# Kernel optimization log

Measured on AMD Instinct MI355X. Metric: run time of the kernel, lower is better.

Reference implementation:

```python
import jax, jax.numpy as jnp
import numpy as np
from jax import lax

B, T, D_IN, H, K, A = 32, 512, 42, 800, 20, 20  # batch, seq, d_in, hidden, linear_out, alphabet_size

def _lstm_dir(x, wih, whh, b, reverse):
    # x: [T,B,D]; wih: [4H,D]; whh: [4H,H]; b: [4H] (b_ih+b_hh merged; mathematically identical)
    xg = jnp.einsum('tbd,hd->tbh', x, wih) + b
    if reverse:
        xg = xg[::-1]
    nh = whh.shape[1]
    h0 = jnp.zeros((x.shape[1], nh), x.dtype)
    def step(carry, xt):
        h, c = carry
        g = xt + h @ whh.T
        i, f, gg, o = jnp.split(g, 4, axis=-1)  # torch gate order i,f,g,o
        c = jax.nn.sigmoid(f) * c + jax.nn.sigmoid(i) * jnp.tanh(gg)
        h = jax.nn.sigmoid(o) * jnp.tanh(c)
        return (h, c), h
    _, hs = lax.scan(step, (h0, h0), xg)
    return hs[::-1] if reverse else hs

_BOND_LENS = jnp.array([145.801, 152.326, 132.868], jnp.float32)  # N-CA, CA-C, C-N (pm)
_BOND_ANGS = jnp.array([2.124, 1.941, 2.028], jnp.float32)

def _coords(tors):
    # tors: [T,B,3] dihedrals -> NeRF-style recursive backbone placement (3 atoms/residue)
    bsz = tors.shape[1]
    a0 = jnp.broadcast_to(jnp.array([0., 0., 1.], jnp.float32), (bsz, 3))
    b0 = jnp.broadcast_to(jnp.array([0., 1., 1.], jnp.float32), (bsz, 3))
    c0 = jnp.broadcast_to(jnp.array([1., 1., 1.], jnp.float32), (bsz, 3))
    def step(carry, tor):
        a, b, c = carry
        outs = []
        for i in range(3):  # three backbone atoms per residue
            r, t, p = _BOND_LENS[i], _BOND_ANGS[i], tor[:, i]
            d2 = jnp.stack([-r * jnp.cos(t) * jnp.ones_like(p),
                            r * jnp.cos(p) * jnp.sin(t),
                            r * jnp.sin(p) * jnp.sin(t)], axis=1)
            bc = c - b
            bc = bc / jnp.linalg.norm(bc, axis=1, keepdims=True)
            n = jnp.cross(b - a, bc)
            n = n / jnp.linalg.norm(n, axis=1, keepdims=True)
            m = jnp.stack([bc, jnp.cross(n, bc), n], axis=2)  # [B,3,3] local frame
            d = jnp.einsum('bij,bj->bi', m, d2) + c
            outs.append(d)
            a, b, c = b, c, d
        return (a, b, c), jnp.stack(outs)
    _, new = lax.scan(step, (a0, b0, c0), tors)  # [T,3,B,3]
    init3 = jnp.stack([a0, b0, c0])
    return jnp.concatenate([init3, new.reshape(-1, bsz, 3)], axis=0)  # [3+3T,B,3]

def _forward(x, wih_l0_f, whh_l0_f, b_l0_f, wih_l0_b, whh_l0_b, b_l0_b,
             wih_l1_f, whh_l1_f, b_l1_f, wih_l1_b, whh_l1_b, b_l1_b,
             lin_w, lin_b, alphabet):
    xs = jnp.transpose(x, (1, 0, 2))  # torch: x.float().transpose(0,1) -> [T,B,D]
    h1 = jnp.concatenate([_lstm_dir(xs, wih_l0_f, whh_l0_f, b_l0_f, False),
                          _lstm_dir(xs, wih_l0_b, whh_l0_b, b_l0_b, True)], axis=-1)
    h2 = jnp.concatenate([_lstm_dir(h1, wih_l1_f, whh_l1_f, b_l1_f, False),
                          _lstm_dir(h1, wih_l1_b, whh_l1_b, b_l1_b, True)], axis=-1)  # [T,B,2H]
    logits = h2 @ lin_w.T + lin_b  # [T,B,K]
    p = jax.nn.softmax(logits, axis=1)  # faithful to nn.Softmax(dim=1) on 3D input (over batch)
    ang = jnp.arctan2(p @ jnp.sin(alphabet), p @ jnp.cos(alphabet))  # [T,B,3] angular mixture
    return _coords(ang)

def setup_inputs():
    key = jax.random.key(0)
    ks = jax.random.split(key, 16)
    s = 0.05
    return {
        'x': jax.random.normal(ks[0], (B, T, D_IN), jnp.float32),
        'wih_l0_f': jax.random.normal(ks[1], (4 * H, D_IN), jnp.float32) * s,
        'whh_l0_f': jax.random.normal(ks[2], (4 * H, H), jnp.float32) * s,
        'b_l0_f': jax.random.normal(ks[3], (4 * H,), jnp.float32) * s,
        'wih_l0_b': jax.random.normal(ks[4], (4 * H, D_IN), jnp.float32) * s,
        'whh_l0_b': jax.random.normal(ks[5], (4 * H, H), jnp.float32) * s,
        'b_l0_b': jax.random.normal(ks[6], (4 * H,), jnp.float32) * s,
        'wih_l1_f': jax.random.normal(ks[7], (4 * H, 2 * H), jnp.float32) * s,
        'whh_l1_f': jax.random.normal(ks[8], (4 * H, H), jnp.float32) * s,
        'b_l1_f': jax.random.normal(ks[9], (4 * H,), jnp.float32) * s,
        'wih_l1_b': jax.random.normal(ks[10], (4 * H, 2 * H), jnp.float32) * s,
        'whh_l1_b': jax.random.normal(ks[11], (4 * H, H), jnp.float32) * s,
        'b_l1_b': jax.random.normal(ks[12], (4 * H,), jnp.float32) * s,
        'lin_w': jax.random.normal(ks[13], (K, 2 * H), jnp.float32) * s,
        'lin_b': jax.random.normal(ks[14], (K,), jnp.float32) * s,
        'alphabet': jax.random.uniform(ks[15], (A, 3), jnp.float32, -np.pi, np.pi),
    }

def reference(x, wih_l0_f, whh_l0_f, b_l0_f, wih_l0_b, whh_l0_b, b_l0_b,
              wih_l1_f, whh_l1_f, b_l1_f, wih_l1_b, whh_l1_b, b_l1_b,
              lin_w, lin_b, alphabet):
    return _forward(x, wih_l0_f, whh_l0_f, b_l0_f, wih_l0_b, whh_l0_b, b_l0_b,
                    wih_l1_f, whh_l1_f, b_l1_f, wih_l1_b, whh_l1_b, b_l1_b,
                    lin_w, lin_b, alphabet)
```

## Files before the change

### kernel.cpp

```cpp
#include <hip/hip_runtime.h>

typedef unsigned short u16;
typedef _Float16 f16x8 __attribute__((ext_vector_type(8)));
typedef float f32x4 __attribute__((ext_vector_type(4)));

#define T_LEN 512
#define BATCH 32
#define DIN 42
#define XPAD 64
#define HID 800
#define G4 3200
#define KCLS 20
#define NBLK 100
#define WSCAN 16
#define HSTR 1664
#define BOFF 832
#define KPAD 1632

__device__ __forceinline__ u16 f2h(float f){
    union { _Float16 h; u16 u; } v; v.h = (_Float16)f; return v.u;
}
__device__ __forceinline__ float sigm(float x){ return 1.f / (1.f + __expf(-x)); }
__device__ __forceinline__ float tanh_(float x){ return 2.f / (1.f + __expf(-2.f * x)) - 1.f; }

__global__ void k_cvt(const float* __restrict__ s, u16* __restrict__ d, int n){
    for (int i = blockIdx.x * blockDim.x + threadIdx.x; i < n; i += gridDim.x * blockDim.x)
        d[i] = f2h(s[i]);
}
__global__ void k_zero16(u16* __restrict__ d, int n){
    for (int i = blockIdx.x * blockDim.x + threadIdx.x; i < n; i += gridDim.x * blockDim.x)
        d[i] = 0;
}
__global__ void k_xT(const float* __restrict__ x, u16* __restrict__ xT){
    const int n = T_LEN * BATCH * XPAD;
    for (int i = blockIdx.x * blockDim.x + threadIdx.x; i < n; i += gridDim.x * blockDim.x){
        int t = i / (BATCH * XPAD);
        int rem = i % (BATCH * XPAD);
        int b = rem / XPAD, k = rem % XPAD;
        xT[i] = (k < DIN) ? f2h(x[((size_t)b * T_LEN + t) * DIN + k]) : (u16)0;
    }
}
__global__ void k_pack2(const float* __restrict__ whh, const float* __restrict__ wih,
                        int nkk, int kin, u16* __restrict__ P2){
    const int n_use = 50 * 2 * nkk * 2 * 64 * 8;
    for (int i = blockIdx.x * blockDim.x + threadIdx.x; i < n_use; i += gridDim.x * blockDim.x){
        int e = i & 7;
        int lane = (i >> 3) & 63;
        int which = (i >> 9) & 1;
        int r = i >> 10;
        int kk = r % nkk;
        int tn = r / nkk;
        int nh = tn & 1, tile = tn >> 1;
        int lr = lane & 15, kgrp = lane >> 4;
        int col = nh * 32 + which * 16 + lr;
        int gate = col >> 4, j = tile * 16 + (col & 15);
        float v;
        if (kk < 25){
            int k = kk * 32 + kgrp * 8 + e;
            v = whh[(size_t)(gate * 800 + j) * 800 + k];
        } else {
            int xk = (kk - 25) * 32 + kgrp * 8 + e;
            v = (xk < kin) ? wih[(size_t)(gate * 800 + j) * kin + xk] : 0.f;
        }
        P2[i] = f2h(v);
    }
}
__global__ void k_pack_bias(const float* __restrict__ b, float* __restrict__ bpk){
    for (int i = blockIdx.x * blockDim.x + threadIdx.x; i < G4; i += gridDim.x * blockDim.x){
        int g = i & 3, j = i >> 2;
        bpk[i] = b[g * 800 + j];
    }
}

__global__ __launch_bounds__(256) void mfma_gemm(
    const u16* __restrict__ A0, const u16* __restrict__ A1, int lda,
    const void* __restrict__ B0_, const void* __restrict__ B1_, int ldb,
    const float* __restrict__ bias0, const float* __restrict__ bias1,
    void* __restrict__ C0, void* __restrict__ C1, int ldc,
    int M, int N, int K, int outmode, int b_is_f32, int khole)
{
    __shared__ u16 At[128 * 40];
    __shared__ u16 Bt[128 * 40];
    const int z = blockIdx.z;
    const u16* Ag = z ? A1 : A0;
    const void* Bg_ = z ? B1_ : B0_;
    const float* bias = z ? bias1 : bias0;
    void* Cg = z ? C1 : C0;
    const u16*   Bu = (const u16*)Bg_;
    const float* Bf = (const float*)Bg_;
    const int tid = threadIdx.x;
    const int lane = tid & 63, w = tid >> 6;
    const int wr = w >> 1, wc = w & 1;
    const int lr = lane & 15, kb8 = (lane >> 4) * 8;
    const int m0 = blockIdx.y * 128, n0 = blockIdx.x * 128;
    const int sr = tid >> 1, skg = (tid & 1) << 4;
    f32x4 acc[4][4] = {};
    const int KT = (K + 31) >> 5;
    for (int kt = 0; kt < KT; ++kt){
        const int k0 = kt << 5;
        __syncthreads();
        {
            size_t base = (size_t)(m0 + sr) * lda + k0 + skg;
            const f16x8* p = (const f16x8*)(Ag + base);
            *(f16x8*)&At[sr * 40 + skg] = p[0];
            *(f16x8*)&At[sr * 40 + skg + 8] = p[1];
        }
        {
            int rn = n0 + sr;
            const int hole = khole && (k0 == 800);
            const int kb = (khole && k0 >= 832) ? (k0 - 32) : k0;
            if (rn < N && !hole && b_is_f32){
                size_t base = (size_t)rn * ldb + kb + skg;
                const float4* p = (const float4*)(Bf + base);
                float4 q0 = p[0], q1 = p[1], q2 = p[2], q3 = p[3];
                f16x8 v0, v1;
                v0[0] = (_Float16)q0.x; v0[1] = (_Float16)q0.y; v0[2] = (_Float16)q0.z; v0[3] = (_Float16)q0.w;
                v0[4] = (_Float16)q1.x; v0[5] = (_Float16)q1.y; v0[6] = (_Float16)q1.z; v0[7] = (_Float16)q1.w;
                v1[0] = (_Float16)q2.x; v1[1] = (_Float16)q2.y; v1[2] = (_Float16)q2.z; v1[3] = (_Float16)q2.w;
                v1[4] = (_Float16)q3.x; v1[5] = (_Float16)q3.y; v1[6] = (_Float16)q3.z; v1[7] = (_Float16)q3.w;
                *(f16x8*)&Bt[sr * 40 + skg] = v0;
                *(f16x8*)&Bt[sr * 40 + skg + 8] = v1;
            } else if (rn < N && !hole){
                size_t base = (size_t)rn * ldb + kb + skg;
                const f16x8* p = (const f16x8*)(Bu + base);
                *(f16x8*)&Bt[sr * 40 + skg] = p[0];
                *(f16x8*)&Bt[sr * 40 + skg + 8] = p[1];
            } else {
                f16x8 zv = {};
                *(f16x8*)&Bt[sr * 40 + skg] = zv;
                *(f16x8*)&Bt[sr * 40 + skg + 8] = zv;
            }
        }
        __syncthreads();
        f16x8 af[4], bfr[4];
        #pragma unroll
        for (int mi = 0; mi < 4; ++mi)
            af[mi] = *(const f16x8*)&At[(wr * 64 + mi * 16 + lr) * 40 + kb8];
        #pragma unroll
        for (int ni = 0; ni < 4; ++ni)
            bfr[ni] = *(const f16x8*)&Bt[(wc * 64 + ni * 16 + lr) * 40 + kb8];
        #pragma unroll
        for (int mi = 0; mi < 4; ++mi)
            #pragma unroll
            for (int ni = 0; ni < 4; ++ni)
                acc[mi][ni] = __builtin_amdgcn_mfma_f32_16x16x32_f16(af[mi], bfr[ni], acc[mi][ni], 0, 0, 0);
    }
    #pragma unroll
    for (int mi = 0; mi < 4; ++mi){
        #pragma unroll
        for (int ni = 0; ni < 4; ++ni){
            int col = n0 + wc * 64 + ni * 16 + lr;
            if (col >= N) continue;
            float bs = bias ? bias[col] : 0.f;
            int pc = (outmode == 2) ? ((col % 800) * 4 + col / 800) : col;
            #pragma unroll
            for (int r = 0; r < 4; ++r){
                int row = m0 + wr * 64 + mi * 16 + ((lane >> 4) * 4 + r);
                float v = acc[mi][ni][r] + bs;
                if (outmode) ((u16*)Cg)[(size_t)row * ldc + pc] = f2h(v);
                else         ((float*)Cg)[(size_t)row * ldc + pc] = v;
            }
        }
    }
}

__global__ __launch_bounds__(256, 1) void scan_coop(
    int nkk, int W, int s0,
    const u16* __restrict__ xTp,
    const u16* __restrict__ xgF, const u16* __restrict__ xgB,
    const u16* __restrict__ P2f, const u16* __restrict__ P2b,
    const float* __restrict__ bpkF, const float* __restrict__ bpkB,
    const u16* __restrict__ hzero, u16* __restrict__ h,
    float* __restrict__ cF, float* __restrict__ cB,
    int cload, int cstore, unsigned* __restrict__ arrive)
{
    __shared__ u16 wlds[2 * 27 * 2 * 64 * 8];
    __shared__ float gLds[32][65];
    const int tid = threadIdx.x;
    const int dir = blockIdx.x & 1;
    const int tile = blockIdx.x >> 1;
    const u16* P2  = dir ? P2b : P2f;
    const u16* xg  = dir ? xgB : xgF;
    const float* bpk = dir ? bpkB : bpkF;
    float* cst = dir ? cB : cF;

    const int wcnt = 2 * nkk * 2 * 64 * 8;
    {
        const u16* src = P2 + (size_t)tile * wcnt;
        for (int i = tid * 8; i < wcnt; i += 256 * 8)
            *(f16x8*)&wlds[i] = *(const f16x8*)&src[i];
    }
    __syncthreads();

    const int lane = tid & 63, w = tid >> 6;
    const int mi = w >> 1, nh = w & 1;
    const int lr = lane & 15, kb8 = (lane >> 4) * 8;
    const int arow = mi * 16 + lr;
    const int b_ep = tid >> 3;
    const int up   = (tid & 7) * 2;
    const int j    = tile * 16 + up;

    float c0 = 0.f, c1 = 0.f;
    if (cload){
        c0 = cst[tile * 512 + tid * 2];
        c1 = cst[tile * 512 + tid * 2 + 1];
    }
    f32x4 bb0 = {}, bb1 = {};
    if (nkk == 27){
        bb0 = *(const f32x4*)(bpk + j * 4);
        bb1 = *(const f32x4*)(bpk + j * 4 + 4);
    }

    const size_t hstep = (size_t)BATCH * HSTR;

    for (int q = 0; q < W; ++q){
        const int s = s0 + q;
        const int t = dir ? (T_LEN - 1 - s) : s;
        const u16* hprev = (s == 0) ? (hzero + dir * BOFF)
                           : (h + (size_t)(dir ? t + 1 : t - 1) * hstep + dir * BOFF);

        const u16* hp = hprev + (size_t)arow * HSTR + kb8;
        f16x8 areg[25];
        #pragma unroll
        for (int kk = 0; kk < 25; ++kk)
            areg[kk] = *(const f16x8*)(hp + kk * 32);
        f16x8 xa0 = {}, xa1 = {}, xv = {};
        if (nkk == 27){
            const u16* xt = xTp + (size_t)t * (BATCH * XPAD) + arow * XPAD + kb8;
            xa0 = *(const f16x8*)(xt);
            xa1 = *(const f16x8*)(xt + 32);
        } else {
            const int qq = dir ? (W - 1 - q) : q;
            xv = *(const f16x8*)(xg + ((size_t)qq * BATCH + b_ep) * G4 + j * 4);
        }

        f32x4 a0a = {}, a0b = {}, a1a = {}, a1b = {};
        #pragma unroll
        for (int kk = 0; kk < 24; kk += 2){
            f16x8 b0e = *(const f16x8*)&wlds[(size_t)((nh * nkk + kk) * 2 + 0) * 512 + lane * 8];
            f16x8 b1e = *(const f16x8*)&wlds[(size_t)((nh * nkk + kk) * 2 + 1) * 512 + lane * 8];
            f16x8 b0o = *(const f16x8*)&wlds[(size_t)((nh * nkk + kk + 1) * 2 + 0) * 512 + lane * 8];
            f16x8 b1o = *(const f16x8*)&wlds[(size_t)((nh * nkk + kk + 1) * 2 + 1) * 512 + lane * 8];
            a0a = __builtin_amdgcn_mfma_f32_16x16x32_f16(areg[kk],     b0e, a0a, 0, 0, 0);
            a1a = __builtin_amdgcn_mfma_f32_16x16x32_f16(areg[kk],     b1e, a1a, 0, 0, 0);
            a0b = __builtin_amdgcn_mfma_f32_16x16x32_f16(areg[kk + 1], b0o, a0b, 0, 0, 0);
            a1b = __builtin_amdgcn_mfma_f32_16x16x32_f16(areg[kk + 1], b1o, a1b, 0, 0, 0);
        }
        {
            f16x8 b0e = *(const f16x8*)&wlds[(size_t)((nh * nkk + 24) * 2 + 0) * 512 + lane * 8];
            f16x8 b1e = *(const f16x8*)&wlds[(size_t)((nh * nkk + 24) * 2 + 1) * 512 + lane * 8];
            a0a = __builtin_amdgcn_mfma_f32_16x16x32_f16(areg[24], b0e, a0a, 0, 0, 0);
            a1a = __builtin_amdgcn_mfma_f32_16x16x32_f16(areg[24], b1e, a1a, 0, 0, 0);
        }
        if (nkk == 27){
            f16x8 b0e = *(const f16x8*)&wlds[(size_t)((nh * nkk + 25) * 2 + 0) * 512 + lane * 8];
            f16x8 b1e = *(const f16x8*)&wlds[(size_t)((nh * nkk + 25) * 2 + 1) * 512 + lane * 8];
            a0b = __builtin_amdgcn_mfma_f32_16x16x32_f16(xa0, b0e, a0b, 0, 0, 0);
            a1b = __builtin_amdgcn_mfma_f32_16x16x32_f16(xa0, b1e, a1b, 0, 0, 0);
            f16x8 b0o = *(const f16x8*)&wlds[(size_t)((nh * nkk + 26) * 2 + 0) * 512 + lane * 8];
            f16x8 b1o = *(const f16x8*)&wlds[(size_t)((nh * nkk + 26) * 2 + 1) * 512 + lane * 8];
            a0a = __builtin_amdgcn_mfma_f32_16x16x32_f16(xa1, b0o, a0a, 0, 0, 0);
            a1a = __builtin_amdgcn_mfma_f32_16x16x32_f16(xa1, b1o, a1a, 0, 0, 0);
        }
        f32x4 acc0 = a0a + a0b;
        f32x4 acc1 = a1a + a1b;
        #pragma unroll
        for (int r = 0; r < 4; ++r){
            int b = mi * 16 + (lane >> 4) * 4 + r;
            gLds[b][nh * 32 + lr]      = acc0[r];
            gLds[b][nh * 32 + 16 + lr] = acc1[r];
        }
        __syncthreads();

        {
            float gi0, gf0, gg0, go0, gi1, gf1, gg1, go1;
            if (nkk == 27){
                gi0 = gLds[b_ep][up]          + bb0[0];
                gf0 = gLds[b_ep][16 + up]     + bb0[1];
                gg0 = gLds[b_ep][32 + up]     + bb0[2];
                go0 = gLds[b_ep][48 + up]     + bb0[3];
                gi1 = gLds[b_ep][up + 1]      + bb1[0];
                gf1 = gLds[b_ep][16 + up + 1] + bb1[1];
                gg1 = gLds[b_ep][32 + up + 1] + bb1[2];
                go1 = gLds[b_ep][48 + up + 1] + bb1[3];
            } else {
                gi0 = gLds[b_ep][up]          + (float)xv[0];
                gf0 = gLds[b_ep][16 + up]     + (float)xv[1];
                gg0 = gLds[b_ep][32 + up]     + (float)xv[2];
                go0 = gLds[b_ep][48 + up]     + (float)xv[3];
                gi1 = gLds[b_ep][up + 1]      + (float)xv[4];
                gf1 = gLds[b_ep][16 + up + 1] + (float)xv[5];
                gg1 = gLds[b_ep][32 + up + 1] + (float)xv[6];
                go1 = gLds[b_ep][48 + up + 1] + (float)xv[7];
            }
            float cn0 = sigm(gf0) * c0 + sigm(gi0) * tanh_(gg0);
            float cn1 = sigm(gf1) * c1 + sigm(gi1) * tanh_(gg1);
            c0 = cn0; c1 = cn1;
            union { unsigned u; _Float16 hh[2]; } pk;
            pk.hh[0] = (_Float16)(sigm(go0) * tanh_(cn0));
            pk.hh[1] = (_Float16)(sigm(go1) * tanh_(cn1));
            unsigned* dst = (unsigned*)(h + (size_t)t * hstep + dir * BOFF + (size_t)b_ep * HSTR + j);
            __hip_atomic_store(dst, pk.u, __ATOMIC_RELAXED, __HIP_MEMORY_SCOPE_AGENT);
        }

        if (q != W - 1){
            const unsigned tgt = (unsigned)(s + 1);
            __syncthreads();
            if (tid == 0)
                __hip_atomic_store(arrive + (size_t)blockIdx.x * 32, tgt,
                                   __ATOMIC_RELAXED, __HIP_MEMORY_SCOPE_AGENT);
            if (tid < 64){
                const unsigned* slot = arrive + (size_t)(((tid < 50) ? tid : 0) * 2 + dir) * 32;
                while (true){
                    unsigned v = __hip_atomic_load(slot, __ATOMIC_RELAXED, __HIP_MEMORY_SCOPE_AGENT);
                    if (__all((int)(v >= tgt))) break;
                    __builtin_amdgcn_s_sleep(1);
                }
            }
            __syncthreads();
        }
    }
    if (cstore){
        cst[tile * 512 + tid * 2]     = c0;
        cst[tile * 512 + tid * 2 + 1] = c1;
    }
}

__global__ __launch_bounds__(64) void k_smax_ang(
    const float* __restrict__ logits, const float* __restrict__ alphabet,
    float* __restrict__ ang)
{
    int t = blockIdx.x;
    __shared__ float P[32][20];
    __shared__ float sA[20][3], cA[20][3];
    int tid = threadIdx.x;
    for (int idx = tid; idx < 32 * 20; idx += 64){
        int b = idx / 20, k = idx % 20;
        P[b][k] = logits[((size_t)t * 32 + b) * 20 + k];
    }
    for (int idx = tid; idx < 60; idx += 64){
        float al = alphabet[idx];
        sA[idx / 3][idx % 3] = sinf(al);
        cA[idx / 3][idx % 3] = cosf(al);
    }
    __syncthreads();
    if (tid < 20){
        float mx = -1e30f;
        for (int b = 0; b < 32; ++b) mx = fmaxf(mx, P[b][tid]);
        float s = 0.f;
        for (int b = 0; b < 32; ++b){ float e = __expf(P[b][tid] - mx); P[b][tid] = e; s += e; }
        float inv = 1.f / s;
        for (int b = 0; b < 32; ++b) P[b][tid] *= inv;
    }
    __syncthreads();
    if (tid < 32){
        float sx = 0, sy = 0, sz = 0, cx = 0, cy = 0, cz = 0;
        for (int k = 0; k < 20; ++k){
            float p = P[tid][k];
            sx += p * sA[k][0]; sy += p * sA[k][1]; sz += p * sA[k][2];
            cx += p * cA[k][0]; cy += p * cA[k][1]; cz += p * cA[k][2];
        }
        size_t base = ((size_t)t * 32 + tid) * 3;
        ang[base + 0] = atan2f(sx, cx);
        ang[base + 1] = atan2f(sy, cy);
        ang[base + 2] = atan2f(sz, cz);
    }
}

__global__ __launch_bounds__(64) void k_coords(const float* __restrict__ ang, float* __restrict__ out){
    int b = threadIdx.x;
    if (b >= 32) return;
    float ax = 0.f, ay = 0.f, az = 1.f;
    float bx = 0.f, by = 1.f, bz = 1.f;
    float cx = 1.f, cy = 1.f, cz = 1.f;
    out[(0 * 32 + b) * 3 + 0] = ax; out[(0 * 32 + b) * 3 + 1] = ay; out[(0 * 32 + b) * 3 + 2] = az;
    out[(1 * 32 + b) * 3 + 0] = bx; out[(1 * 32 + b) * 3 + 1] = by; out[(1 * 32 + b) * 3 + 2] = bz;
    out[(2 * 32 + b) * 3 + 0] = cx; out[(2 * 32 + b) * 3 + 1] = cy; out[(2 * 32 + b) * 3 + 2] = cz;
    const float rr[3] = {145.801f, 152.326f, 132.868f};
    const float ba[3] = {2.124f, 1.941f, 2.028f};
    float ct[3], st[3];
    #pragma unroll
    for (int i = 0; i < 3; ++i){ ct[i] = cosf(ba[i]); st[i] = sinf(ba[i]); }
    for (int t = 0; t < T_LEN; ++t){
        #pragma unroll
        for (int i = 0; i < 3; ++i){
            float p = ang[((size_t)t * 32 + b) * 3 + i];
            float d2x = -rr[i] * ct[i];
            float d2y = rr[i] * cosf(p) * st[i];
            float d2z = rr[i] * sinf(p) * st[i];
            float bcx = cx - bx, bcy = cy - by, bcz = cz - bz;
            float inb = 1.f / sqrtf(bcx * bcx + bcy * bcy + bcz * bcz);
            bcx *= inb; bcy *= inb; bcz *= inb;
            float ux = bx - ax, uy = by - ay, uz = bz - az;
            float nx = uy * bcz - uz * bcy;
            float ny = uz * bcx - ux * bcz;
            float nz = ux * bcy - uy * bcx;
            float inn = 1.f / sqrtf(nx * nx + ny * ny + nz * nz);
            nx *= inn; ny *= inn; nz *= inn;
            float mx = ny * bcz - nz * bcy;
            float my = nz * bcx - nx * bcz;
            float mz = nx * bcy - ny * bcx;
            float dx = bcx * d2x + mx * d2y + nx * d2z + cx;
            float dy = bcy * d2x + my * d2y + ny * d2z + cy;
            float dz = bcz * d2x + mz * d2y + nz * d2z + cz;
            int row = 3 + t * 3 + i;
            out[((size_t)row * 32 + b) * 3 + 0] = dx;
            out[((size_t)row * 32 + b) * 3 + 1] = dy;
            out[((size_t)row * 32 + b) * 3 + 2] = dz;
            ax = bx; ay = by; az = bz;
            bx = cx; by = cy; bz = cz;
            cx = dx; cy = dy; cz = dz;
        }
    }
}

extern "C" void kernel_launch(void* const* d_in, const int* in_sizes, int n_in,
                              void* d_out, int out_size, void* d_ws, size_t ws_size,
                              hipStream_t stream)
{
    const float* x     = (const float*)d_in[0];
    const float* wih0f = (const float*)d_in[1];
    const float* whh0f = (const float*)d_in[2];
    const float* b0f   = (const float*)d_in[3];
    const float* wih0b = (const float*)d_in[4];
    const float* whh0b = (const float*)d_in[5];
    const float* b0b   = (const float*)d_in[6];
    const float* wih1f = (const float*)d_in[7];
    const float* whh1f = (const float*)d_in[8];
    const float* b1f   = (const float*)d_in[9];
    const float* wih1b = (const float*)d_in[10];
    const float* whh1b = (const float*)d_in[11];
    const float* b1b   = (const float*)d_in[12];
    const float* linw  = (const float*)d_in[13];
    const float* linb  = (const float*)d_in[14];
    const float* alpha = (const float*)d_in[15];
    (void)in_sizes; (void)n_in; (void)out_size; (void)ws_size;

    char* ws = (char*)d_ws;
    size_t off = 0;
    auto alloc = [&](size_t bytes) -> void* {
        off = (off + 255) & ~(size_t)255;
        void* p = ws + off;
        off += bytes;
        return p;
    };
    u16* xT     = (u16*)alloc((size_t)T_LEN * BATCH * XPAD * 2);
    u16* h1     = (u16*)alloc((size_t)T_LEN * BATCH * HSTR * 2);
    u16* h2     = (u16*)alloc((size_t)T_LEN * BATCH * HSTR * 2);
    u16* P2_0f  = (u16*)alloc((size_t)50 * 2 * 27 * 2 * 64 * 8 * 2);
    u16* P2_0b  = (u16*)alloc((size_t)50 * 2 * 27 * 2 * 64 * 8 * 2);
    u16* P2_1f  = (u16*)alloc((size_t)50 * 2 * 25 * 2 * 64 * 8 * 2);
    u16* P2_1b  = (u16*)alloc((size_t)50 * 2 * 25 * 2 * 64 * 8 * 2);
    u16* linwB  = (u16*)alloc((size_t)KCLS * 1600 * 2);
    float* bpk0f = (float*)alloc((size_t)G4 * 4);
    float* bpk0b = (float*)alloc((size_t)G4 * 4);
    u16* hzero  = (u16*)alloc((size_t)BATCH * HSTR * 2);
    float* c1f  = (float*)alloc((size_t)50 * 512 * 4);
    float* c1b  = (float*)alloc((size_t)50 * 512 * 4);
    u16* xgFc   = (u16*)alloc((size_t)WSCAN * BATCH * G4 * 2);
    u16* xgBc   = (u16*)alloc((size_t)WSCAN * BATCH * G4 * 2);
    unsigned* arrive = (unsigned*)alloc((size_t)NBLK * 32 * 4);
    float* logitsF = (float*)xgFc;
    float* angF    = (float*)xgBc;

    k_zero16<<<dim3(32), dim3(256), 0, stream>>>(hzero, BATCH * HSTR);
    k_cvt<<<dim3(64), dim3(256), 0, stream>>>(linw, linwB, KCLS * 1600);
    k_xT<<<dim3(512), dim3(256), 0, stream>>>(x, xT);
    k_pack2<<<dim3(1024), dim3(256), 0, stream>>>(whh0f, wih0f, 27, DIN, P2_0f);
    k_pack2<<<dim3(1024), dim3(256), 0, stream>>>(whh0b, wih0b, 27, DIN, P2_0b);
    k_pack2<<<dim3(1024), dim3(256), 0, stream>>>(whh1f, nullptr, 25, 0, P2_1f);
    k_pack2<<<dim3(1024), dim3(256), 0, stream>>>(whh1b, nullptr, 25, 0, P2_1b);
    k_pack_bias<<<dim3(8), dim3(256), 0, stream>>>(b0f, bpk0f);
    k_pack_bias<<<dim3(8), dim3(256), 0, stream>>>(b0b, bpk0b);

    const size_t hstep = (size_t)BATCH * HSTR;

    hipMemsetAsync(arrive, 0, (size_t)NBLK * 32 * 4, stream);
    scan_coop<<<dim3(NBLK), dim3(256), 0, stream>>>(
        27, T_LEN, 0,
        xT, nullptr, nullptr,
        P2_0f, P2_0b, bpk0f, bpk0b,
        hzero, h1, nullptr, nullptr, 0, 0, arrive);

    hipMemsetAsync(arrive, 0, (size_t)NBLK * 32 * 4, stream);
    for (int w = 0; w < T_LEN / WSCAN; ++w){
        const int s0  = w * WSCAN;
        const int t0f = s0;
        const int t0b = T_LEN - (w + 1) * WSCAN;
        mfma_gemm<<<dim3(G4 / 128, WSCAN * BATCH / 128, 2), dim3(256), 0, stream>>>(
            h1 + (size_t)t0f * hstep, h1 + (size_t)t0b * hstep, HSTR,
            wih1f, wih1b, 1600, b1f, b1b,
            xgFc, xgBc, G4, WSCAN * BATCH, G4, KPAD, 2, 1, 1);
        scan_coop<<<dim3(NBLK), dim3(256), 0, stream>>>(
            25, WSCAN, s0,
            nullptr, xgFc, xgBc,
            P2_1f, P2_1b, nullptr, nullptr,
            hzero, h2, c1f, c1b, (w > 0) ? 1 : 0, 1, arrive);
    }

    mfma_gemm<<<dim3(1, T_LEN * BATCH / 128, 1), dim3(256), 0, stream>>>(
        h2, h2, HSTR, linwB, linwB, 1600, linb, linb,
        logitsF, logitsF, KCLS, T_LEN * BATCH, KCLS, KPAD, 0, 0, 1);

    k_smax_ang<<<dim3(T_LEN), dim3(64), 0, stream>>>(logitsF, alpha, angF);
    k_coords<<<dim3(1), dim3(64), 0, stream>>>(angF, (float*)d_out);
}
```

Baseline: 8.163 ms.

## Fuse layer-1 input projection into a single persistent 200-block scan kernel

Replaces the layer-1 loop, which alternated a windowed input-projection GEMM with short cooperative scan launches, with one persistent kernel. The new kernel keeps both the recurrent and input weights for 8 hidden units per block resident in LDS and computes the h1 projection inside each step before waiting on the barrier. It uses 200 blocks instead of 100, cutting per-block recurrent work and letting the h1 part overlap the cross-block wait. In exchange it launches many fewer kernels, but each step now does three times the MFMA work in the loop and the flag barrier has to span more blocks.

Result: slower. 9.063 ms (+11.0%).

```diff
diff --git a/kernel.cpp b/kernel.cpp
--- a/kernel.cpp
+++ b/kernel.cpp
@@ -12,7 +12,6 @@
 #define G4 3200
 #define KCLS 20
 #define NBLK 100
-#define WSCAN 16
 #define HSTR 1664
 #define BOFF 832
 #define KPAD 1632
@@ -62,6 +61,28 @@
             int xk = (kk - 25) * 32 + kgrp * 8 + e;
             v = (xk < kin) ? wih[(size_t)(gate * 800 + j) * kin + xk] : 0.f;
         }
+        P2[i] = f2h(v);
+    }
+}
+__global__ void k_pack_l1(const float* __restrict__ whh1, const float* __restrict__ wih1,
+                          u16* __restrict__ P2){
+    const int n = 100 * 2 * 75 * 512;
+    for (int i = blockIdx.x * blockDim.x + threadIdx.x; i < n; i += gridDim.x * blockDim.x){
+        int e = i & 7;
+        int lane = (i >> 3) & 63;
+        int rem = i >> 9;
+        int kk = rem % 75;
+        int r = rem / 75;
+        int wv = r & 1, tile = r >> 1;
+        int lr = lane & 15, kgrp = lane >> 4;
+        int col = wv * 16 + lr;
+        int g = col & 3, u = col >> 2;
+        int j = tile * 8 + u;
+        int krel = kgrp * 8 + e;
+        float v;
+        if (kk < 25)      v = whh1[(size_t)(g * 800 + j) * 800 + kk * 32 + krel];
+        else if (kk < 50) v = wih1[(size_t)(g * 800 + j) * 1600 + (kk - 25) * 32 + krel];
+        else              v = wih1[(size_t)(g * 800 + j) * 1600 + 800 + (kk - 50) * 32 + krel];
         P2[i] = f2h(v);
     }
 }
@@ -167,12 +188,10 @@
 __global__ __launch_bounds__(256, 1) void scan_coop(
     int nkk, int W, int s0,
     const u16* __restrict__ xTp,
-    const u16* __restrict__ xgF, const u16* __restrict__ xgB,
     const u16* __restrict__ P2f, const u16* __restrict__ P2b,
     const float* __restrict__ bpkF, const float* __restrict__ bpkB,
     const u16* __restrict__ hzero, u16* __restrict__ h,
-    float* __restrict__ cF, float* __restrict__ cB,
-    int cload, int cstore, unsigned* __restrict__ arrive)
+    unsigned* __restrict__ arrive)
 {
     __shared__ u16 wlds[2 * 27 * 2 * 64 * 8];
     __shared__ float gLds[32][65];
@@ -180,9 +199,7 @@
     const int dir = blockIdx.x & 1;
     const int tile = blockIdx.x >> 1;
     const u16* P2  = dir ? P2b : P2f;
-    const u16* xg  = dir ? xgB : xgF;
     const float* bpk = dir ? bpkB : bpkF;
-    float* cst = dir ? cB : cF;
 
     const int wcnt = 2 * nkk * 2 * 64 * 8;
     {
@@ -201,15 +218,8 @@
     const int j    = tile * 16 + up;
 
     float c0 = 0.f, c1 = 0.f;
-    if (cload){
-        c0 = cst[tile * 512 + tid * 2];
-        c1 = cst[tile * 512 + tid * 2 + 1];
-    }
-    f32x4 bb0 = {}, bb1 = {};
-    if (nkk == 27){
-        bb0 = *(const f32x4*)(bpk + j * 4);
-        bb1 = *(const f32x4*)(bpk + j * 4 + 4);
-    }
+    f32x4 bb0 = *(const f32x4*)(bpk + j * 4);
+    f32x4 bb1 = *(const f32x4*)(bpk + j * 4 + 4);
 
     const size_t hstep = (size_t)BATCH * HSTR;
 
@@ -224,14 +234,11 @@
         #pragma unroll
         for (int kk = 0; kk < 25; ++kk)
             areg[kk] = *(const f16x8*)(hp + kk * 32);
-        f16x8 xa0 = {}, xa1 = {}, xv = {};
-        if (nkk == 27){
+        f16x8 xa0, xa1;
+        {
             const u16* xt = xTp + (size_t)t * (BATCH * XPAD) + arow * XPAD + kb8;
             xa0 = *(const f16x8*)(xt);
             xa1 = *(const f16x8*)(xt + 32);
-        } else {
-            const int qq = dir ? (W - 1 - q) : q;
-            xv = *(const f16x8*)(xg + ((size_t)qq * BATCH + b_ep) * G4 + j * 4);
         }
 
         f32x4 a0a = {}, a0b = {}, a1a = {}, a1b = {};
@@ -252,7 +259,7 @@
             a0a = __builtin_amdgcn_mfma_f32_16x16x32_f16(areg[24], b0e, a0a, 0, 0, 0);
             a1a = __builtin_amdgcn_mfma_f32_16x16x32_f16(areg[24], b1e, a1a, 0, 0, 0);
         }
-        if (nkk == 27){
+        {
             f16x8 b0e = *(const f16x8*)&wlds[(size_t)((nh * nkk + 25) * 2 + 0) * 512 + lane * 8];
             f16x8 b1e = *(const f16x8*)&wlds[(size_t)((nh * nkk + 25) * 2 + 1) * 512 + lane * 8];
             a0b = __builtin_amdgcn_mfma_f32_16x16x32_f16(xa0, b0e, a0b, 0, 0, 0);
@@ -273,26 +280,14 @@
         __syncthreads();
 
         {
-            float gi0, gf0, gg0, go0, gi1, gf1, gg1, go1;
-            if (nkk == 27){
-                gi0 = gLds[b_ep][up]          + bb0[0];
-                gf0 = gLds[b_ep][16 + up]     + bb0[1];
-                gg0 = gLds[b_ep][32 + up]     + bb0[2];
-                go0 = gLds[b_ep][48 + up]     + bb0[3];
-                gi1 = gLds[b_ep][up + 1]      + bb1[0];
-                gf1 = gLds[b_ep][16 + up + 1] + bb1[1];
-                gg1 = gLds[b_ep][32 + up + 1] + bb1[2];
-                go1 = gLds[b_ep][48 + up + 1] + bb1[3];
-            } else {
-                gi0 = gLds[b_ep][up]          + (float)xv[0];
-                gf0 = gLds[b_ep][16 + up]     + (float)xv[1];
-                gg0 = gLds[b_ep][32 + up]     + (float)xv[2];
-                go0 = gLds[b_ep][48 + up]     + (float)xv[3];
-                gi1 = gLds[b_ep][up + 1]      + (float)xv[4];
-                gf1 = gLds[b_ep][16 + up + 1] + (float)xv[5];
-                gg1 = gLds[b_ep][32 + up + 1] + (float)xv[6];
-                go1 = gLds[b_ep][48 + up + 1] + (float)xv[7];
-            }
+            float gi0 = gLds[b_ep][up]          + bb0[0];
+            float gf0 = gLds[b_ep][16 + up]     + bb0[1];
+            float gg0 = gLds[b_ep][32 + up]     + bb0[2];
+            float go0 = gLds[b_ep][48 + up]     + bb0[3];
+            float gi1 = gLds[b_ep][up + 1]      + bb1[0];
+            float gf1 = gLds[b_ep][16 + up + 1] + bb1[1];
+            float gg1 = gLds[b_ep][32 + up + 1] + bb1[2];
+            float go1 = gLds[b_ep][48 + up + 1] + bb1[3];
             float cn0 = sigm(gf0) * c0 + sigm(gi0) * tanh_(gg0);
             float cn1 = sigm(gf1) * c1 + sigm(gi1) * tanh_(gg1);
             c0 = cn0; c1 = cn1;
@@ -320,9 +315,114 @@
             __syncthreads();
         }
     }
-    if (cstore){
-        cst[tile * 512 + tid * 2]     = c0;
-        cst[tile * 512 + tid * 2 + 1] = c1;
+}
+
+__global__ __launch_bounds__(256, 1) void scan_l1(
+    const u16* __restrict__ P2f, const u16* __restrict__ P2b,
+    const float* __restrict__ bpkF, const float* __restrict__ bpkB,
+    const u16* __restrict__ h1, const u16* __restrict__ hzero,
+    u16* __restrict__ h2, unsigned* __restrict__ arrive)
+{
+    __shared__ u16 wlds[2 * 75 * 512];
+    __shared__ float gLds[32][36];
+    const int tid = threadIdx.x;
+    const int dir = blockIdx.x & 1;
+    const int tile = blockIdx.x >> 1;
+    const u16* P2 = dir ? P2b : P2f;
+    const float* bpk = dir ? bpkB : bpkF;
+
+    {
+        const u16* src = P2 + (size_t)tile * (2 * 75 * 512);
+        for (int i = tid * 8; i < 2 * 75 * 512; i += 256 * 8)
+            *(f16x8*)&wlds[i] = *(const f16x8*)&src[i];
+    }
+    __syncthreads();
+
+    const int lane = tid & 63, w = tid >> 6;
+    const int mi = w >> 1, wv = w & 1;
+    const int lr = lane & 15, kb8 = (lane >> 4) * 8;
+    const int arow = mi * 16 + lr;
+    const int b_ep = tid >> 3, u_ep = tid & 7;
+    const int j = tile * 8 + u_ep;
+    const f32x4 bb = *(const f32x4*)(bpk + j * 4);
+    float cc = 0.f;
+    const size_t hstep = (size_t)BATCH * HSTR;
+    const u16* wl = wlds + (size_t)wv * 75 * 512 + (size_t)lane * 8;
+
+    for (int s = 0; s < T_LEN; ++s){
+        const int t = dir ? (T_LEN - 1 - s) : s;
+        f32x4 aA = {}, aB = {};
+        const u16* h1row = h1 + (size_t)t * hstep + (size_t)arow * HSTR;
+        {
+            f16x8 a[25];
+            #pragma unroll
+            for (int k = 0; k < 25; ++k) a[k] = *(const f16x8*)(h1row + k * 32 + kb8);
+            #pragma unroll
+            for (int k = 0; k < 25; ++k){
+                f16x8 bw = *(const f16x8*)(wl + (size_t)(25 + k) * 512);
+                if (k & 1) aB = __builtin_amdgcn_mfma_f32_16x16x32_f16(a[k], bw, aB, 0, 0, 0);
+                else       aA = __builtin_amdgcn_mfma_f32_16x16x32_f16(a[k], bw, aA, 0, 0, 0);
+            }
+        }
+        {
+            f16x8 a[25];
+            #pragma unroll
+            for (int k = 0; k < 25; ++k) a[k] = *(const f16x8*)(h1row + BOFF + k * 32 + kb8);
+            #pragma unroll
+            for (int k = 0; k < 25; ++k){
+                f16x8 bw = *(const f16x8*)(wl + (size_t)(50 + k) * 512);
+                if (k & 1) aB = __builtin_amdgcn_mfma_f32_16x16x32_f16(a[k], bw, aB, 0, 0, 0);
+                else       aA = __builtin_amdgcn_mfma_f32_16x16x32_f16(a[k], bw, aA, 0, 0, 0);
+            }
+        }
+        if (s > 0){
+            const unsigned tgt = (unsigned)s;
+            if (tid < 128){
+                int slot = (tid < 100) ? tid : 99;
+                const unsigned* sp = arrive + (size_t)(slot * 2 + dir) * 32;
+                while (true){
+                    unsigned v = __hip_atomic_load(sp, __ATOMIC_RELAXED, __HIP_MEMORY_SCOPE_AGENT);
+                    if (__all((int)(v >= tgt))) break;
+                    __builtin_amdgcn_s_sleep(1);
+                }
+            }
+            __syncthreads();
+        }
+        {
+            const u16* hp = (s == 0) ? (hzero + dir * BOFF + (size_t)arow * HSTR)
+                : (h2 + (size_t)(dir ? t + 1 : t - 1) * hstep + dir * BOFF + (size_t)arow * HSTR);
+            f16x8 a[25];
+            #pragma unroll
+            for (int k = 0; k < 25; ++k) a[k] = *(const f16x8*)(hp + k * 32 + kb8);
+            #pragma unroll
+            for (int k = 0; k < 25; ++k){
+                f16x8 bw = *(const f16x8*)(wl + (size_t)k * 512);
+                if (k & 1) aB = __builtin_amdgcn_mfma_f32_16x16x32_f16(a[k], bw, aB, 0, 0, 0);
+                else       aA = __builtin_amdgcn_mfma_f32_16x16x32_f16(a[k], bw, aA, 0, 0, 0);
+            }
+        }
+        f32x4 acc = aA + aB;
+        #pragma unroll
+        for (int r = 0; r < 4; ++r)
+            gLds[mi * 16 + (lane >> 4) * 4 + r][wv * 16 + lr] = acc[r];
+        __syncthreads();
+        {
+            float gi = gLds[b_ep][u_ep * 4 + 0] + bb[0];
+            float gf = gLds[b_ep][u_ep * 4 + 1] + bb[1];
+            float gg = gLds[b_ep][u_ep * 4 + 2] + bb[2];
+            float go = gLds[b_ep][u_ep * 4 + 3] + bb[3];
+            float cn = sigm(gf) * cc + sigm(gi) * tanh_(gg);
+            cc = cn;
+            u16 hv = f2h(sigm(go) * tanh_(cn));
+            u16* dst = h2 + (size_t)t * hstep + dir * BOFF + (size_t)b_ep * HSTR + j;
+            __hip_atomic_store(dst, hv, __ATOMIC_RELAXED, __HIP_MEMORY_SCOPE_AGENT);
+        }
+        if (s != T_LEN - 1){
+            __syncthreads();
+            if (tid == 0)
+                __hip_atomic_store(arrive + (size_t)blockIdx.x * 32, (unsigned)(s + 1),
+                                   __ATOMIC_RELAXED, __HIP_MEMORY_SCOPE_AGENT);
+        }
     }
 }
 
@@ -444,59 +544,43 @@
         off += bytes;
         return p;
     };
-    u16* xT     = (u16*)alloc((size_t)T_LEN * BATCH * XPAD * 2);
-    u16* h1     = (u16*)alloc((size_t)T_LEN * BATCH * HSTR * 2);
-    u16* h2     = (u16*)alloc((size_t)T_LEN * BATCH * HSTR * 2);
-    u16* P2_0f  = (u16*)alloc((size_t)50 * 2 * 27 * 2 * 64 * 8 * 2);
-    u16* P2_0b  = (u16*)alloc((size_t)50 * 2 * 27 * 2 * 64 * 8 * 2);
-    u16* P2_1f  = (u16*)alloc((size_t)50 * 2 * 25 * 2 * 64 * 8 * 2);
-    u16* P2_1b  = (u16*)alloc((size_t)50 * 2 * 25 * 2 * 64 * 8 * 2);
+    u16* xT   = (u16*)alloc((size_t)T_LEN * BATCH * XPAD * 2);
+    u16* h1   = (u16*)alloc((size_t)T_LEN * BATCH * HSTR * 2);
+    u16* h2   = (u16*)alloc((size_t)T_LEN * BATCH * HSTR * 2);
+    u16* Wbig = (u16*)alloc((size_t)2 * 7680000 * 2);
+    u16* P2_0f  = Wbig;
+    u16* P2_0b  = Wbig + 2764800;
+    u16* P2L1f  = Wbig;
+    u16* P2L1b  = Wbig + 7680000;
     u16* linwB  = (u16*)alloc((size_t)KCLS * 1600 * 2);
     float* bpk0f = (float*)alloc((size_t)G4 * 4);
     float* bpk0b = (float*)alloc((size_t)G4 * 4);
+    float* bpk1f = (float*)alloc((size_t)G4 * 4);
+    float* bpk1b = (float*)alloc((size_t)G4 * 4);
     u16* hzero  = (u16*)alloc((size_t)BATCH * HSTR * 2);
-    float* c1f  = (float*)alloc((size_t)50 * 512 * 4);
-    float* c1b  = (float*)alloc((size_t)50 * 512 * 4);
-    u16* xgFc   = (u16*)alloc((size_t)WSCAN * BATCH * G4 * 2);
-    u16* xgBc   = (u16*)alloc((size_t)WSCAN * BATCH * G4 * 2);
-    unsigned* arrive = (unsigned*)alloc((size_t)NBLK * 32 * 4);
-    float* logitsF = (float*)xgFc;
-    float* angF    = (float*)xgBc;
+    unsigned* arrive = (unsigned*)alloc((size_t)256 * 32 * 4);
+    float* logitsF = (float*)Wbig;
+    float* angF    = (float*)(Wbig + 8000000);
 
     k_zero16<<<dim3(32), dim3(256), 0, stream>>>(hzero, BATCH * HSTR);
     k_cvt<<<dim3(64), dim3(256), 0, stream>>>(linw, linwB, KCLS * 1600);
     k_xT<<<dim3(512), dim3(256), 0, stream>>>(x, xT);
     k_pack2<<<dim3(1024), dim3(256), 0, stream>>>(whh0f, wih0f, 27, DIN, P2_0f);
     k_pack2<<<dim3(1024), dim3(256), 0, stream>>>(whh0b, wih0b, 27, DIN, P2_0b);
-    k_pack2<<<dim3(1024), dim3(256), 0, stream>>>(whh1f, nullptr, 25, 0, P2_1f);
-    k_pack2<<<dim3(1024), dim3(256), 0, stream>>>(whh1b, nullptr, 25, 0, P2_1b);
     k_pack_bias<<<dim3(8), dim3(256), 0, stream>>>(b0f, bpk0f);
     k_pack_bias<<<dim3(8), dim3(256), 0, stream>>>(b0b, bpk0b);
-
-    const size_t hstep = (size_t)BATCH * HSTR;
-
-    hipMemsetAsync(arrive, 0, (size_t)NBLK * 32 * 4, stream);
+    k_pack_bias<<<dim3(8), dim3(256), 0, stream>>>(b1f, bpk1f);
+    k_pack_bias<<<dim3(8), dim3(256), 0, stream>>>(b1b, bpk1b);
+
+    hipMemsetAsync(arrive, 0, (size_t)256 * 32 * 4, stream);
     scan_coop<<<dim3(NBLK), dim3(256), 0, stream>>>(
-        27, T_LEN, 0,
-        xT, nullptr, nullptr,
-        P2_0f, P2_0b, bpk0f, bpk0b,
-        hzero, h1, nullptr, nullptr, 0, 0, arrive);
-
-    hipMemsetAsync(arrive, 0, (size_t)NBLK * 32 * 4, stream);
-    for (int w = 0; w < T_LEN / WSCAN; ++w){
-        const int s0  = w * WSCAN;
-        const int t0f = s0;
-        const int t0b = T_LEN - (w + 1) * WSCAN;
-        mfma_gemm<<<dim3(G4 / 128, WSCAN * BATCH / 128, 2), dim3(256), 0, stream>>>(
-            h1 + (size_t)t0f * hstep, h1 + (size_t)t0b * hstep, HSTR,
-            wih1f, wih1b, 1600, b1f, b1b,
-            xgFc, xgBc, G4, WSCAN * BATCH, G4, KPAD, 2, 1, 1);
-        scan_coop<<<dim3(NBLK), dim3(256), 0, stream>>>(
-            25, WSCAN, s0,
-            nullptr, xgFc, xgBc,
-            P2_1f, P2_1b, nullptr, nullptr,
-            hzero, h2, c1f, c1b, (w > 0) ? 1 : 0, 1, arrive);
-    }
+        27, T_LEN, 0, xT, P2_0f, P2_0b, bpk0f, bpk0b, hzero, h1, arrive);
+
+    k_pack_l1<<<dim3(2048), dim3(256), 0, stream>>>(whh1f, wih1f, P2L1f);
+    k_pack_l1<<<dim3(2048), dim3(256), 0, stream>>>(whh1b, wih1b, P2L1b);
+    hipMemsetAsync(arrive, 0, (size_t)256 * 32 * 4, stream);
+    scan_l1<<<dim3(200), dim3(256), 0, stream>>>(
+        P2L1f, P2L1b, bpk1f, bpk1b, h1, hzero, h2, arrive);
 
     mfma_gemm<<<dim3(1, T_LEN * BATCH / 128, 1), dim3(256), 0, stream>>>(
         h2, h2, HSTR, linwB, linwB, 1600, linb, linb,
```
